# Optimization experiments

Measured on AMD Instinct MI355X. Metric: run time of the kernel, lower is better.

## Reference

```python
import jax, jax.numpy as jnp
import numpy as np

G = 13            # grid_size
A = 5             # num_anchors
C = 36            # num_classes
OBJ_SCALE = 5.0
NOOBJ_SCALE = 1.0
CLASS_SCALE = 1.0
COORD_SCALE = 1.0
ANCHORS = jnp.array([[1.08, 1.19], [3.42, 4.41], [6.63, 11.38], [9.42, 5.11], [16.62, 10.52]], dtype=jnp.float32)


def setup_inputs() -> dict:
    key = jax.random.key(0)
    k1, k2, k3 = jax.random.split(key, 3)
    B, T = 1024, 30
    predictions = jax.random.normal(k1, (B, A * (5 + C), G, G), dtype=jnp.float32)
    # x,y,w,h normalized to (0,1); class id in [0,C) stored as float in channel 4
    xywh = jax.random.uniform(k2, (B, T, 4), dtype=jnp.float32, minval=1e-3, maxval=0.999)
    cls = jax.random.randint(k3, (B, T, 1), 0, C).astype(jnp.float32)
    target = jnp.concatenate([xywh, cls], axis=-1)
    return {"predictions": predictions, "target": target}


def build_targets(target):
    # target: [B, T, 5]  (x, y, w, h, class), x/y/w/h in [0,1)
    B, T, _ = target.shape
    valid = jnp.sum(target, axis=-1) != 0                      # [B, T]
    gx = target[..., 0] * G
    gy = target[..., 1] * G
    gw = target[..., 2] * G
    gh = target[..., 3] * G
    gi = gx.astype(jnp.int32)                                  # int() truncation (values >= 0)
    gj = gy.astype(jnp.int32)
    # anchor IoU for boxes centered at origin: inter = min(w)*min(h)
    aw = ANCHORS[:, 0]                                          # [A]
    ah = ANCHORS[:, 1]
    inter = jnp.minimum(gw[..., None], aw) * jnp.minimum(gh[..., None], ah)   # [B,T,A]
    union = (gw * gh)[..., None] + aw * ah - inter
    iou = inter / (union + 1e-16)
    best_n = jnp.argmax(iou, axis=-1)                           # [B, T] first-max, matches torch loop
    baw = ANCHORS[best_n, 0]
    bah = ANCHORS[best_n, 1]
    tx = gx - gi.astype(gx.dtype)
    ty = gy - gj.astype(gy.dtype)
    tw = jnp.log(gw / baw + 1e-16)
    th = jnp.log(gh / bah + 1e-16)
    cls_idx = target[..., 4].astype(jnp.int32)                  # [B, T]

    N = B * A * G * G
    b_idx = jnp.arange(B, dtype=jnp.int32)[:, None]             # [B,1] -> broadcast to [B,T]
    flat = ((b_idx * A + best_n.astype(jnp.int32)) * G + gj) * G + gi   # [B,T]
    flat = jnp.where(valid, flat, N)                            # out-of-bounds -> dropped
    flat = flat.reshape(-1)                                     # [B*T]

    conf_mask = jnp.full((N,), NOOBJ_SCALE, dtype=jnp.float32).at[flat].set(OBJ_SCALE, mode="drop")
    coord_mask = jnp.zeros((N, 4), dtype=jnp.float32).at[flat].set(1.0, mode="drop")
    class_mask = jnp.zeros((N, C), dtype=jnp.float32).at[flat].set(CLASS_SCALE, mode="drop")
    tconf = jnp.zeros((N,), dtype=jnp.float32).at[flat].set(1.0, mode="drop")
    tcoord_vals = jnp.stack([tx, ty, tw, th], axis=-1).reshape(-1, 4)
    tcoord = jnp.zeros((N, 4), dtype=jnp.float32).at[flat].set(tcoord_vals, mode="drop")
    tclass = jnp.zeros((N, C), dtype=jnp.float32).at[flat, cls_idx.reshape(-1)].set(1.0, mode="drop")

    shp = (B, A, G, G)
    return (coord_mask.reshape(shp + (4,)), conf_mask.reshape(shp), class_mask.reshape(shp + (C,)),
            tcoord.reshape(shp + (4,)), tconf.reshape(shp), tclass.reshape(shp + (C,)))


def reference(predictions, target):
    B = predictions.shape[0]
    p = predictions.reshape(B, A, 5 + C, G, G).transpose(0, 1, 3, 4, 2)   # [B,A,G,G,5+C]
    coord_mask, conf_mask, class_mask, tcoord, tconf, tclass = build_targets(target)
    pred_coord = p[..., 1:5]
    pred_conf = jax.nn.sigmoid(p[..., 0])
    pred_class = p[..., 5:]
    loss_coord = COORD_SCALE * jnp.sum((pred_coord * coord_mask - tcoord * coord_mask) ** 2) / B
    loss_conf = jnp.sum((pred_conf * conf_mask - tconf * conf_mask) ** 2) / B
    labels = jnp.argmax(tclass.reshape(-1, C), axis=1)
    logp = jax.nn.log_softmax(pred_class.reshape(-1, C), axis=-1)
    loss_class = CLASS_SCALE * (-jnp.take_along_axis(logp, labels[:, None], axis=1).sum()) / B
    total_loss = loss_coord + loss_conf + loss_class
    return (total_loss, loss_coord, loss_conf, loss_class)
```

## Files before the change

kernel.cpp:

```cpp
#include <hip/hip_runtime.h>

#define GQ 13
#define AQ 5
#define CQ 36
#define TQ 30
#define CH (5 + CQ)
#define GG (GQ * GQ)
#define CELLS (AQ * GG)
#define BLOCK 256
#define BPI 4


__global__ __launch_bounds__(BLOCK, 6) void yolo_cells(
    const float* __restrict__ pred,
    const float* __restrict__ target,
    float* __restrict__ ws, int nb)
{
    __shared__ int   s_pack[TQ];
    __shared__ float s_tc[TQ][4];
    __shared__ float s_red[3][BLOCK / 64];

    const int b   = blockIdx.y;
    const int tid = threadIdx.x;
    const int n   = blockIdx.x * BLOCK + tid;
    const bool act = (n < CELLS);
    const int nc  = act ? n : (CELLS - 1);
    const int a   = nc / GG;
    const int r   = nc - a * GG;
    const float* base = pred + ((size_t)(b * AQ + a) * CH) * GG + r;

    float tg0 = 0.f, tg1 = 0.f, tg2 = 0.f, tg3 = 0.f, tg4 = 0.f;
    if (tid < TQ) {
        const float* tg = target + ((size_t)b * TQ + tid) * 5;
        tg0 = tg[0]; tg1 = tg[1]; tg2 = tg[2]; tg3 = tg[3]; tg4 = tg[4];
    }

    float p0 = __builtin_nontemporal_load(base);
    float v[CQ];
    #pragma unroll
    for (int c = 0; c < CQ; c++)
        v[c] = __builtin_nontemporal_load(base + (size_t)(5 + c) * GG);

    __builtin_amdgcn_sched_barrier(0);

    if (tid < TQ) {
        bool valid = (tg0 + tg1 + tg2 + tg3 + tg4) != 0.0f;
        float gx = tg0 * GQ, gy = tg1 * GQ, gw = tg2 * GQ, gh = tg3 * GQ;
        int gi = (int)gx, gj = (int)gy;
        const float AW[5] = {1.08f, 3.42f, 6.63f, 9.42f, 16.62f};
        const float AH[5] = {1.19f, 4.41f, 11.38f, 5.11f, 10.52f};
        float best = -1.0f; int bn = 0;
        #pragma unroll
        for (int k = 0; k < AQ; k++) {
            float inter = fminf(gw, AW[k]) * fminf(gh, AH[k]);
            float un    = gw * gh + AW[k] * AH[k] - inter;
            float iou   = inter / (un + 1e-16f);
            if (iou > best) { best = iou; bn = k; }
        }
        int cell = (bn * GQ + gj) * GQ + gi;
        s_pack[tid]  = valid ? ((cell << 6) | (int)tg4) : -1;
        s_tc[tid][0] = gx - (float)gi;
        s_tc[tid][1] = gy - (float)gj;
        s_tc[tid][2] = __logf(gw / AW[bn] + 1e-16f);
        s_tc[tid][3] = __logf(gh / AH[bn] + 1e-16f);
    }
    __syncthreads();

    float lcoord = 0.0f, lconf = 0.0f, lclass = 0.0f;
    if (act) {
        int mt = -1, minc = 63;
        #pragma unroll
        for (int t = 0; t < TQ; t++) {
            int p = s_pack[t];
            if ((p >> 6) == n) { mt = t; minc = min(minc, p & 63); }
        }
        bool obj = (mt >= 0);
        int lab  = obj ? minc : 0;

        float sig = 1.0f / (1.0f + __expf(-p0));
        float d   = obj ? 5.0f * (sig - 1.0f) : sig;
        lconf = d * d;

        if (obj) {
            float d1 = __builtin_nontemporal_load(base + 1 * GG) - s_tc[mt][0];
            float d2 = __builtin_nontemporal_load(base + 2 * GG) - s_tc[mt][1];
            float d3 = __builtin_nontemporal_load(base + 3 * GG) - s_tc[mt][2];
            float d4 = __builtin_nontemporal_load(base + 4 * GG) - s_tc[mt][3];
            lcoord = d1 * d1 + d2 * d2 + d3 * d3 + d4 * d4;
        }

        float sum = 0.0f, vl = 0.0f;
        #pragma unroll
        for (int c = 0; c < CQ; c++) {
            sum += __expf(v[c]);
            vl = (c == lab) ? v[c] : vl;
        }
        lclass = __logf(sum) - vl;
    }

    #pragma unroll
    for (int off = 32; off > 0; off >>= 1) {
        lcoord += __shfl_down(lcoord, off, 64);
        lconf  += __shfl_down(lconf,  off, 64);
        lclass += __shfl_down(lclass, off, 64);
    }
    int wv = tid >> 6, ln = tid & 63;
    if (ln == 0) { s_red[0][wv] = lcoord; s_red[1][wv] = lconf; s_red[2][wv] = lclass; }
    __syncthreads();
    if (tid == 0) {
        float a0 = 0.f, a1 = 0.f, a2 = 0.f;
        #pragma unroll
        for (int w = 0; w < BLOCK / 64; w++) {
            a0 += s_red[0][w]; a1 += s_red[1][w]; a2 += s_red[2][w];
        }
        int bid = b * BPI + blockIdx.x;
        ws[0 * nb + bid] = a0;
        ws[1 * nb + bid] = a1;
        ws[2 * nb + bid] = a2;
    }
}

__global__ __launch_bounds__(BLOCK) void yolo_reduce(
    const float* __restrict__ ws, float* __restrict__ out, int nb, float invB)
{
    __shared__ float s_red[3][BLOCK / 64];
    const int tid = threadIdx.x;
    float a0 = 0.f, a1 = 0.f, a2 = 0.f;
    for (int i = tid; i < nb; i += BLOCK) {
        a0 += ws[0 * nb + i];
        a1 += ws[1 * nb + i];
        a2 += ws[2 * nb + i];
    }
    #pragma unroll
    for (int off = 32; off > 0; off >>= 1) {
        a0 += __shfl_down(a0, off, 64);
        a1 += __shfl_down(a1, off, 64);
        a2 += __shfl_down(a2, off, 64);
    }
    int wv = tid >> 6, ln = tid & 63;
    if (ln == 0) { s_red[0][wv] = a0; s_red[1][wv] = a1; s_red[2][wv] = a2; }
    __syncthreads();
    if (tid == 0) {
        float r0 = 0.f, r1 = 0.f, r2 = 0.f;
        #pragma unroll
        for (int w = 0; w < BLOCK / 64; w++) {
            r0 += s_red[0][w]; r1 += s_red[1][w]; r2 += s_red[2][w];
        }
        r0 *= invB; r1 *= invB; r2 *= invB;
        out[0] = r0 + r1 + r2;
        out[1] = r0;
        out[2] = r1;
        out[3] = r2;
    }
}

extern "C" void kernel_launch(void* const* d_in, const int* in_sizes, int n_in,
                              void* d_out, int out_size, void* d_ws, size_t ws_size,
                              hipStream_t stream)
{
    const float* pred   = (const float*)d_in[0];
    const float* target = (const float*)d_in[1];
    float* out = (float*)d_out;
    float* ws  = (float*)d_ws;

    int B  = in_sizes[0] / (AQ * CH * GG);
    int nb = B * BPI;

    dim3 grid(BPI, B);
    yolo_cells<<<grid, BLOCK, 0, stream>>>(pred, target, ws, nb);
    yolo_reduce<<<1, BLOCK, 0, stream>>>(ws, out, nb, 1.0f / (float)B);
}
```

Baseline: 201.3 us.

## Process four cells per thread with vector loads, one block per image

Each thread now handles four consecutive grid cells and loads each channel as a 4-wide vector instead of one scalar, so one 256-thread block covers a whole image instead of four blocks. The tail cell group per anchor overlaps and is masked so only the last element counts. The aim is fewer load instructions, fewer blocks and a smaller reduction workspace. In exchange, registers per thread rise sharply (36 float4 values), which can cut occupancy, and the float4 loads have only 4-byte alignment.

```diff
diff --git a/kernel.cpp b/kernel.cpp
--- a/kernel.cpp
+++ b/kernel.cpp
@@ -7,11 +7,14 @@
 #define CH (5 + CQ)
 #define GG (GQ * GQ)
 #define CELLS (AQ * GG)
+#define JPP 43
+#define ACT (AQ * JPP)
 #define BLOCK 256
-#define BPI 4
+
+typedef float float4a __attribute__((ext_vector_type(4), aligned(4)));
 
 
-__global__ __launch_bounds__(BLOCK, 6) void yolo_cells(
+__global__ __launch_bounds__(BLOCK) void yolo_cells4(
     const float* __restrict__ pred,
     const float* __restrict__ target,
     float* __restrict__ ws, int nb)
@@ -20,14 +23,17 @@
     __shared__ float s_tc[TQ][4];
     __shared__ float s_red[3][BLOCK / 64];
 
-    const int b   = blockIdx.y;
+    const int b   = blockIdx.x;
     const int tid = threadIdx.x;
-    const int n   = blockIdx.x * BLOCK + tid;
-    const bool act = (n < CELLS);
-    const int nc  = act ? n : (CELLS - 1);
-    const int a   = nc / GG;
-    const int r   = nc - a * GG;
-    const float* base = pred + ((size_t)(b * AQ + a) * CH) * GG + r;
+
+    const bool on = (tid < ACT);
+    const int ts  = on ? tid : 0;
+    const int a   = ts / JPP;
+    const int j   = ts - a * JPP;
+    const bool tail = (j == JPP - 1);
+    const int r0  = tail ? (GG - 4) : (j * 4);
+    const int c0  = a * GG + r0;
+    const float* base = pred + (size_t)((b * AQ + a) * CH) * GG + r0;
 
     float tg0 = 0.f, tg1 = 0.f, tg2 = 0.f, tg3 = 0.f, tg4 = 0.f;
     if (tid < TQ) {
@@ -35,11 +41,11 @@
         tg0 = tg[0]; tg1 = tg[1]; tg2 = tg[2]; tg3 = tg[3]; tg4 = tg[4];
     }
 
-    float p0 = __builtin_nontemporal_load(base);
-    float v[CQ];
+    float4a p0 = __builtin_nontemporal_load((const float4a*)base);
+    float4a w[CQ];
     #pragma unroll
     for (int c = 0; c < CQ; c++)
-        v[c] = __builtin_nontemporal_load(base + (size_t)(5 + c) * GG);
+        w[c] = __builtin_nontemporal_load((const float4a*)(base + (size_t)(5 + c) * GG));
 
     __builtin_amdgcn_sched_barrier(0);
 
@@ -67,35 +73,50 @@
     __syncthreads();
 
     float lcoord = 0.0f, lconf = 0.0f, lclass = 0.0f;
-    if (act) {
-        int mt = -1, minc = 63;
+    if (on) {
+        float actm[4];
+        #pragma unroll
+        for (int e = 0; e < 4; e++) actm[e] = (!tail || e == 3) ? 1.0f : 0.0f;
+
+        int mt[4]   = {-1, -1, -1, -1};
+        int minc[4] = {63, 63, 63, 63};
         #pragma unroll
         for (int t = 0; t < TQ; t++) {
             int p = s_pack[t];
-            if ((p >> 6) == n) { mt = t; minc = min(minc, p & 63); }
-        }
-        bool obj = (mt >= 0);
-        int lab  = obj ? minc : 0;
-
-        float sig = 1.0f / (1.0f + __expf(-p0));
-        float d   = obj ? 5.0f * (sig - 1.0f) : sig;
-        lconf = d * d;
-
-        if (obj) {
-            float d1 = __builtin_nontemporal_load(base + 1 * GG) - s_tc[mt][0];
-            float d2 = __builtin_nontemporal_load(base + 2 * GG) - s_tc[mt][1];
-            float d3 = __builtin_nontemporal_load(base + 3 * GG) - s_tc[mt][2];
-            float d4 = __builtin_nontemporal_load(base + 4 * GG) - s_tc[mt][3];
-            lcoord = d1 * d1 + d2 * d2 + d3 * d3 + d4 * d4;
+            int d = (p >> 6) - c0;
+            #pragma unroll
+            for (int e = 0; e < 4; e++)
+                if (d == e) { mt[e] = t; minc[e] = min(minc[e], p & 63); }
         }
 
-        float sum = 0.0f, vl = 0.0f;
+        float cf[4] = {p0.x, p0.y, p0.z, p0.w};
         #pragma unroll
-        for (int c = 0; c < CQ; c++) {
-            sum += __expf(v[c]);
-            vl = (c == lab) ? v[c] : vl;
+        for (int e = 0; e < 4; e++) {
+            bool obj = (mt[e] >= 0);
+            int lab  = obj ? minc[e] : 0;
+
+            float sig = 1.0f / (1.0f + __expf(-cf[e]));
+            float d   = obj ? 5.0f * (sig - 1.0f) : sig;
+            lconf += actm[e] * d * d;
+
+            if (obj && actm[e] != 0.0f) {
+                int t = mt[e];
+                float d1 = __builtin_nontemporal_load(base + 1 * GG + e) - s_tc[t][0];
+                float d2 = __builtin_nontemporal_load(base + 2 * GG + e) - s_tc[t][1];
+                float d3 = __builtin_nontemporal_load(base + 3 * GG + e) - s_tc[t][2];
+                float d4 = __builtin_nontemporal_load(base + 4 * GG + e) - s_tc[t][3];
+                lcoord += d1 * d1 + d2 * d2 + d3 * d3 + d4 * d4;
+            }
+
+            float sum = 0.0f, vl = 0.0f;
+            #pragma unroll
+            for (int c = 0; c < CQ; c++) {
+                float vv = w[c][e];
+                sum += __expf(vv);
+                vl = (c == lab) ? vv : vl;
+            }
+            lclass += actm[e] * (__logf(sum) - vl);
         }
-        lclass = __logf(sum) - vl;
     }
 
     #pragma unroll
@@ -110,13 +131,12 @@
     if (tid == 0) {
         float a0 = 0.f, a1 = 0.f, a2 = 0.f;
         #pragma unroll
-        for (int w = 0; w < BLOCK / 64; w++) {
-            a0 += s_red[0][w]; a1 += s_red[1][w]; a2 += s_red[2][w];
+        for (int w2 = 0; w2 < BLOCK / 64; w2++) {
+            a0 += s_red[0][w2]; a1 += s_red[1][w2]; a2 += s_red[2][w2];
         }
-        int bid = b * BPI + blockIdx.x;
-        ws[0 * nb + bid] = a0;
-        ws[1 * nb + bid] = a1;
-        ws[2 * nb + bid] = a2;
+        ws[0 * nb + b] = a0;
+        ws[1 * nb + b] = a1;
+        ws[2 * nb + b] = a2;
     }
 }
 
@@ -164,9 +184,8 @@
     float* ws  = (float*)d_ws;
 
     int B  = in_sizes[0] / (AQ * CH * GG);
-    int nb = B * BPI;
+    int nb = B;
 
-    dim3 grid(BPI, B);
-    yolo_cells<<<grid, BLOCK, 0, stream>>>(pred, target, ws, nb);
+    yolo_cells4<<<B, BLOCK, 0, stream>>>(pred, target, ws, nb);
     yolo_reduce<<<1, BLOCK, 0, stream>>>(ws, out, nb, 1.0f / (float)B);
 }
```

New measurement: 203.6 us. About the same (+1.2%).
